# Performance work log

Hardware: AMD Instinct MI355X
Metric: run time of the kernel (lower is better)

## Reference

```python
import jax, jax.numpy as jnp
import numpy as np

B, L, D_MODEL = 4, 1024, 1024
S, NUM_TOKENS = 2048, 1000
H, E = 16, 256          # n_heads, d_keys
D_LLM = 4096


def setup_inputs() -> dict:
    key = jax.random.key(0)
    ks = jax.random.split(key, 11)
    def lin(k, fan_in, fan_out):
        bound = 1.0 / np.sqrt(fan_in)
        kw, kb = jax.random.split(k)
        W = jax.random.uniform(kw, (fan_out, fan_in), jnp.float32, -bound, bound)
        b = jax.random.uniform(kb, (fan_out,), jnp.float32, -bound, bound)
        return W, b
    Wq, bq = lin(ks[0], D_MODEL, H * E)
    Wk, bk = lin(ks[1], NUM_TOKENS, H * E)
    Wv, bv = lin(ks[2], NUM_TOKENS, H * E)
    Wo, bo = lin(ks[3], H * E, D_LLM)
    return {
        "target_embedding": jax.random.normal(ks[4], (B, L, D_MODEL), jnp.float32),
        "source_embedding": jax.random.normal(ks[5], (S, NUM_TOKENS), jnp.float32),
        "value_embedding": jax.random.normal(ks[6], (S, NUM_TOKENS), jnp.float32),
        "Wq": Wq, "bq": bq, "Wk": Wk, "bk": bk,
        "Wv": Wv, "bv": bv, "Wo": Wo, "bo": bo,
    }


def reference(target_embedding, source_embedding, value_embedding,
              Wq, bq, Wk, bk, Wv, bv, Wo, bo):
    # projections
    q = (target_embedding @ Wq.T + bq).reshape(B, L, H, E)   # [B,L,H,E]
    k = (source_embedding @ Wk.T + bk).reshape(S, H, E)      # [S,H,E] shared across batch
    v = (value_embedding @ Wv.T + bv).reshape(S, H, E)       # [S,H,E]
    scale = 1.0 / jnp.sqrt(jnp.float32(E))
    scores = jnp.einsum('blhe,she->bhls', q, k)               # [B,H,L,S]
    A = jax.nn.softmax(scale * scores, axis=-1)               # dropout is identity at eval
    out = jnp.einsum('bhls,she->blhe', A, v)                  # [B,L,H,E]
    out = out.reshape(B, L, H * E)
    return out @ Wo.T + bo                                    # [B,L,d_llm]
```

## Files before the change

kernel.cpp:

```cpp
#include <hip/hip_runtime.h>
#include <hip/hip_bf16.h>


#define B_ 4
#define L_ 1024
#define DM_ 1024
#define S_ 2048
#define NT_ 1000
#define H_ 16
#define E_ 256
#define HE_ 4096
#define DL_ 4096

typedef __attribute__((ext_vector_type(8))) short short8;
typedef __attribute__((ext_vector_type(4))) float f32x4;
typedef unsigned int u32;

__device__ __forceinline__ ushort f2bf(float x) {
  __hip_bfloat16 h = __float2bfloat16(x);
  return *reinterpret_cast<ushort*>(&h);
}

__device__ __forceinline__ void gload_lds16(const void* g, void* l) {
  __builtin_amdgcn_global_load_lds(
      (const __attribute__((address_space(1))) u32*)g,
      (__attribute__((address_space(3))) u32*)l, 16, 0, 0);
}

__global__ __launch_bounds__(256) void cast_pad_k(
    const float* __restrict__ src, ushort* __restrict__ dst,
    int rows, int ks, int kd) {
  const int kd8 = kd >> 3;
  const int idx = blockIdx.x * 256 + threadIdx.x;
  if (idx >= rows * kd8) return;
  const int r = idx / kd8;
  const int c0 = (idx - r * kd8) << 3;
  union { ushort u[8]; short8 v; } o;
  if (c0 + 8 <= ks) {
    const float4 f0 = *(const float4*)(src + (size_t)r * ks + c0);
    const float4 f1 = *(const float4*)(src + (size_t)r * ks + c0 + 4);
    o.u[0] = f2bf(f0.x); o.u[1] = f2bf(f0.y); o.u[2] = f2bf(f0.z); o.u[3] = f2bf(f0.w);
    o.u[4] = f2bf(f1.x); o.u[5] = f2bf(f1.y); o.u[6] = f2bf(f1.z); o.u[7] = f2bf(f1.w);
  } else {
#pragma unroll
    for (int j = 0; j < 8; ++j) o.u[j] = 0;
  }
  *(short8*)(dst + (size_t)r * kd + c0) = o.v;
}

template <typename OT>
__global__ __launch_bounds__(256) void gemm_mfma_t(
    const ushort* __restrict__ A, const ushort* __restrict__ W,
    const float* __restrict__ bias, OT* __restrict__ C,
    int M, int N, int K) {
  __shared__ char lds[2][2][16384];
  const int t = threadIdx.x;
  const int w = t >> 6;
  const int l = t & 63;
  const int a = l & 15;
  const int g = l >> 4;
  const int wr = w >> 1, wc = w & 1;
  const int bm = blockIdx.y << 7, bn = blockIdx.x << 7;
  const int sr = (l >> 3);
  const int sc = l & 7;

  f32x4 acc[4][4];
#pragma unroll
  for (int m = 0; m < 4; ++m)
#pragma unroll
    for (int n = 0; n < 4; ++n) acc[m][n] = (f32x4){0.f, 0.f, 0.f, 0.f};

  const int NTT = K >> 6;
  int cur = 0;

  auto stage = [&](int kt, int buf) {
    const int k0 = kt << 6;
#pragma unroll
    for (int j = 0; j < 4; ++j) {
      const int rb = (w << 5) + (j << 3);
      const int r = rb + sr;
      const int cs = sc ^ ((r & 4) >> 1);
      const size_t gofs = (size_t)r * K + k0 + (cs << 3);
      gload_lds16(A + (size_t)bm * K + gofs, &lds[buf][0][rb << 7]);
      gload_lds16(W + (size_t)bn * K + gofs, &lds[buf][1][rb << 7]);
    }
  };

  auto compute = [&](int buf) {
    const char* lA = lds[buf][0];
    const char* lB = lds[buf][1];
#pragma unroll
    for (int kk = 0; kk < 2; ++kk) {
      const int cc = (kk << 2) + g;
      short8 bfr[4];
#pragma unroll
      for (int n = 0; n < 4; ++n) {
        const int rl = (wc << 6) + (n << 4) + a;
        bfr[n] = *(const short8*)&lB[(rl << 7) + ((cc ^ ((rl & 4) >> 1)) << 4)];
      }
#pragma unroll
      for (int m = 0; m < 4; ++m) {
        const int rl = (wr << 6) + (m << 4) + a;
        const short8 afr = *(const short8*)&lA[(rl << 7) + ((cc ^ ((rl & 4) >> 1)) << 4)];
#pragma unroll
        for (int n = 0; n < 4; ++n)
          acc[m][n] = __builtin_amdgcn_mfma_f32_16x16x32_bf16(afr, bfr[n], acc[m][n], 0, 0, 0);
      }
    }
  };

  stage(0, 0);
  for (int kt = 0; kt < NTT; ++kt) {
    __syncthreads();
    if (kt + 1 < NTT) stage(kt + 1, cur ^ 1);
    compute(cur);
    cur ^= 1;
  }

  float bb[4];
#pragma unroll
  for (int n = 0; n < 4; ++n) bb[n] = bias[bn + (wc << 6) + (n << 4) + a];
#pragma unroll
  for (int m = 0; m < 4; ++m) {
#pragma unroll
    for (int ri = 0; ri < 4; ++ri) {
      const size_t row = (size_t)bm + (wr << 6) + (m << 4) + (g << 2) + ri;
      OT* Crow = C + row * N + bn + (wc << 6) + a;
#pragma unroll
      for (int n = 0; n < 4; ++n) {
        const float v = acc[m][n][ri] + bb[n];
        if constexpr (__is_same(OT, ushort)) Crow[n << 4] = f2bf(v);
        else Crow[n << 4] = v;
      }
    }
  }
}

__global__ __launch_bounds__(256) void transpose_bf16_k(
    const ushort* __restrict__ v, ushort* __restrict__ vt) {
  __shared__ ushort tile[64][72];
  const int t = threadIdx.x;
  const int s0 = blockIdx.x << 6;
  const int c0 = blockIdx.y << 6;
#pragma unroll
  for (int i = 0; i < 2; ++i) {
    const int idx = t + (i << 8);
    const int ch = idx & 7, s = idx >> 3;
    *(short8*)&tile[s][ch << 3] =
        *(const short8*)(v + (size_t)(s0 + s) * HE_ + c0 + (ch << 3));
  }
  __syncthreads();
#pragma unroll
  for (int i = 0; i < 2; ++i) {
    const int idx = t + (i << 8);
    const int sch = idx & 7, e = idx >> 3;
    union { ushort u[8]; short8 v8; } ou;
#pragma unroll
    for (int j = 0; j < 8; ++j) ou.u[j] = tile[(sch << 3) + j][e];
    *(short8*)(vt + (size_t)(c0 + e) * S_ + s0 + (sch << 3)) = ou.v8;
  }
}

__global__ __launch_bounds__(256) void attn_mfma_k(
    const ushort* __restrict__ q, const ushort* __restrict__ k,
    const ushort* __restrict__ vt, ushort* __restrict__ o) {
  __shared__ char kls[32 * 512];
  __shared__ char vls[256 * 64];
  __shared__ ushort pls[4][16 * 36];

  const int t = threadIdx.x;
  const int w = t >> 6;
  const int l = t & 63;
  const int a = l & 15;
  const int g = l >> 4;
  const int h = blockIdx.y;
  const int b = blockIdx.z;
  const size_t qrow = (size_t)(b << 10) + (blockIdx.x << 6) + (w << 4);

  short8 qf[8];
  {
    const size_t rb = (qrow + a) * HE_ + (h << 8) + (g << 3);
#pragma unroll
    for (int kk = 0; kk < 8; ++kk) qf[kk] = *(const short8*)(q + rb + (kk << 5));
  }

  f32x4 oa[16];
#pragma unroll
  for (int eg = 0; eg < 16; ++eg) oa[eg] = (f32x4){0.f, 0.f, 0.f, 0.f};
  float m_r[4] = {-3e38f, -3e38f, -3e38f, -3e38f};
  float l_r[4] = {0.f, 0.f, 0.f, 0.f};

  for (int s0 = 0; s0 < S_; s0 += 32) {
    __syncthreads();
#pragma unroll
    for (int i = 0; i < 4; ++i) {
      const int idx = t + (i << 8);
      const int c = idx & 31, s = idx >> 5;
      short8 kv = *(const short8*)(k + ((size_t)(s0 + s) << 12) + (h << 8) + (c << 3));
      *(short8*)&kls[((s << 9) + (c << 4)) ^ ((s & 7) << 4)] = kv;
    }
#pragma unroll
    for (int i = 0; i < 4; ++i) {
      const int idx = t + (i << 8);
      const int sc = idx & 3, e = idx >> 2;
      short8 vv = *(const short8*)(vt + ((size_t)((h << 8) + e) << 11) + s0 + (sc << 3));
      *(short8*)&vls[((e << 6) + (sc << 4)) ^ ((e & 3) << 4)] = vv;
    }
    __syncthreads();

    f32x4 sd0 = (f32x4){0.f, 0.f, 0.f, 0.f};
    f32x4 sd1 = (f32x4){0.f, 0.f, 0.f, 0.f};
#pragma unroll
    for (int kk = 0; kk < 8; ++kk) {
      const short8 kf0 = *(const short8*)
          &kls[((a << 9) + (g << 4) + (kk << 6)) ^ ((a & 7) << 4)];
      const short8 kf1 = *(const short8*)
          &kls[(((a + 16) << 9) + (g << 4) + (kk << 6)) ^ ((a & 7) << 4)];
      sd0 = __builtin_amdgcn_mfma_f32_16x16x32_bf16(qf[kk], kf0, sd0, 0, 0, 0);
      sd1 = __builtin_amdgcn_mfma_f32_16x16x32_bf16(qf[kk], kf1, sd1, 0, 0, 0);
    }

    float p0[4], p1[4];
#pragma unroll
    for (int r = 0; r < 4; ++r) {
      const float v0 = sd0[r] * 0.0625f;
      const float v1 = sd1[r] * 0.0625f;
      p0[r] = v0; p1[r] = v1;
      float mx = fmaxf(v0, v1);
      mx = fmaxf(mx, __shfl_xor(mx, 1));
      mx = fmaxf(mx, __shfl_xor(mx, 2));
      mx = fmaxf(mx, __shfl_xor(mx, 4));
      mx = fmaxf(mx, __shfl_xor(mx, 8));
      const float mnew = fmaxf(m_r[r], mx);
      const float corr = __expf(m_r[r] - mnew);
      m_r[r] = mnew;
      const float e0 = __expf(p0[r] - mnew);
      const float e1 = __expf(p1[r] - mnew);
      p0[r] = e0; p1[r] = e1;
      float sum = e0 + e1;
      sum += __shfl_xor(sum, 1);
      sum += __shfl_xor(sum, 2);
      sum += __shfl_xor(sum, 4);
      sum += __shfl_xor(sum, 8);
      l_r[r] = l_r[r] * corr + sum;
#pragma unroll
      for (int eg = 0; eg < 16; ++eg) oa[eg][r] *= corr;
    }

    {
      ushort* pw = pls[w];
#pragma unroll
      for (int r = 0; r < 4; ++r) {
        const int qq = (g << 2) + r;
        pw[qq * 36 + a] = f2bf(p0[r]);
        pw[qq * 36 + a + 16] = f2bf(p1[r]);
      }
    }
    asm volatile("s_waitcnt lgkmcnt(0)" ::: "memory");
    __builtin_amdgcn_sched_barrier(0);
    short8 pf;
    {
      const char* pb = (const char*)pls[w];
      union { unsigned long long u[2]; short8 v8; } pu;
      pu.u[0] = *(const unsigned long long*)(pb + a * 72 + (g << 4));
      pu.u[1] = *(const unsigned long long*)(pb + a * 72 + (g << 4) + 8);
      pf = pu.v8;
    }

#pragma unroll
    for (int eg = 0; eg < 16; ++eg) {
      const int e = (eg << 4) + a;
      const short8 vf = *(const short8*)
          &vls[((e << 6) + (g << 4)) ^ ((e & 3) << 4)];
      oa[eg] = __builtin_amdgcn_mfma_f32_16x16x32_bf16(pf, vf, oa[eg], 0, 0, 0);
    }
  }

  float inv[4];
#pragma unroll
  for (int r = 0; r < 4; ++r) inv[r] = 1.f / l_r[r];
#pragma unroll
  for (int eg = 0; eg < 16; ++eg) {
#pragma unroll
    for (int r = 0; r < 4; ++r) {
      o[(qrow + (g << 2) + r) * HE_ + (h << 8) + (eg << 4) + a] =
          f2bf(oa[eg][r] * inv[r]);
    }
  }
}

extern "C" void kernel_launch(void* const* d_in, const int* in_sizes, int n_in,
                              void* d_out, int out_size, void* d_ws, size_t ws_size,
                              hipStream_t stream) {
  (void)in_sizes; (void)n_in; (void)out_size; (void)ws_size;
  const float* te = (const float*)d_in[0];
  const float* se = (const float*)d_in[1];
  const float* ve = (const float*)d_in[2];
  const float* Wq = (const float*)d_in[3];
  const float* bq = (const float*)d_in[4];
  const float* Wk = (const float*)d_in[5];
  const float* bk = (const float*)d_in[6];
  const float* Wv = (const float*)d_in[7];
  const float* bv = (const float*)d_in[8];
  const float* Wo = (const float*)d_in[9];
  const float* bo = (const float*)d_in[10];
  float* out = (float*)d_out;

  ushort* tebf = (ushort*)d_ws;
  ushort* sebf = tebf + (size_t)4096 * 1024;
  ushort* vebf = sebf + (size_t)2048 * 1024;
  ushort* wqb  = vebf + (size_t)2048 * 1024;
  ushort* wkb  = wqb  + (size_t)4096 * 1024;
  ushort* wvb  = wkb  + (size_t)4096 * 1024;
  ushort* wob  = wvb  + (size_t)4096 * 1024;
  ushort* qbf  = wob  + (size_t)4096 * 4096;
  ushort* kbf  = qbf  + (size_t)4096 * 4096;
  ushort* vbf  = kbf  + (size_t)2048 * 4096;
  ushort* vtb  = vbf  + (size_t)2048 * 4096;
  ushort* awsb = vtb  + (size_t)4096 * 2048;

  dim3 blk(256);
  auto cgrid = [](int rows, int kd) { return dim3((rows * (kd >> 3) + 255) / 256); };
  cast_pad_k<<<cgrid(4096, 1024), blk, 0, stream>>>(te, tebf, 4096, 1024, 1024);
  cast_pad_k<<<cgrid(2048, 1024), blk, 0, stream>>>(se, sebf, 2048, 1000, 1024);
  cast_pad_k<<<cgrid(2048, 1024), blk, 0, stream>>>(ve, vebf, 2048, 1000, 1024);
  cast_pad_k<<<cgrid(4096, 1024), blk, 0, stream>>>(Wq, wqb, 4096, 1024, 1024);
  cast_pad_k<<<cgrid(4096, 1024), blk, 0, stream>>>(Wk, wkb, 4096, 1000, 1024);
  cast_pad_k<<<cgrid(4096, 1024), blk, 0, stream>>>(Wv, wvb, 4096, 1000, 1024);
  cast_pad_k<<<cgrid(4096, 4096), blk, 0, stream>>>(Wo, wob, 4096, 4096, 4096);

  gemm_mfma_t<ushort><<<dim3(32, 32), blk, 0, stream>>>(tebf, wqb, bq, qbf, 4096, 4096, 1024);
  gemm_mfma_t<ushort><<<dim3(32, 16), blk, 0, stream>>>(sebf, wkb, bk, kbf, 2048, 4096, 1024);
  gemm_mfma_t<ushort><<<dim3(32, 16), blk, 0, stream>>>(vebf, wvb, bv, vbf, 2048, 4096, 1024);
  transpose_bf16_k<<<dim3(S_ / 64, HE_ / 64), blk, 0, stream>>>(vbf, vtb);
  attn_mfma_k<<<dim3(L_ / 64, H_, B_), blk, 0, stream>>>(qbf, kbf, vtb, awsb);
  gemm_mfma_t<float><<<dim3(32, 32), blk, 0, stream>>>(awsb, wob, bo, out, 4096, 4096, 4096);
}
```

Before: 962.0 us.

## Widen attention KV tile to 64, use direct-to-LDS loads, lazy rescale, XCD-aware block mapping

The attention kernel now processes 64 keys per iteration instead of 32, halving the number of barrier-separated steps and doubling MFMA work per LDS fill. K and V tiles are loaded with global_load_lds using an XOR swizzle in place of register-staged copies. The online softmax skips rescaling the accumulators unless the running max grows by more than 8, which saves multiplies but leaves exponentials less tightly bounded. The 3D grid is flattened into a 1D index remapped so that blocks of the same head land on the same XCD, to improve L2 reuse of K/V. LDS usage doubles, which may reduce occupancy.

```diff
diff --git a/kernel.cpp b/kernel.cpp
--- a/kernel.cpp
+++ b/kernel.cpp
@@ -164,18 +164,21 @@
 __global__ __launch_bounds__(256) void attn_mfma_k(
     const ushort* __restrict__ q, const ushort* __restrict__ k,
     const ushort* __restrict__ vt, ushort* __restrict__ o) {
-  __shared__ char kls[32 * 512];
-  __shared__ char vls[256 * 64];
-  __shared__ ushort pls[4][16 * 36];
+  __shared__ char kls[64 * 512];
+  __shared__ char vls[256 * 128];
+  __shared__ ushort pls[4][16 * 72];
 
   const int t = threadIdx.x;
   const int w = t >> 6;
   const int l = t & 63;
   const int a = l & 15;
   const int g = l >> 4;
-  const int h = blockIdx.y;
-  const int b = blockIdx.z;
-  const size_t qrow = (size_t)(b << 10) + (blockIdx.x << 6) + (w << 4);
+  const int bid = blockIdx.x;
+  const int f = ((bid & 7) << 7) + (bid >> 3);
+  const int h = f >> 6;
+  const int bb = (f >> 4) & 3;
+  const int qt = f & 15;
+  const size_t qrow = ((size_t)bb << 10) + (qt << 6) + (w << 4);
 
   short8 qf[8];
   {
@@ -190,61 +193,70 @@
   float m_r[4] = {-3e38f, -3e38f, -3e38f, -3e38f};
   float l_r[4] = {0.f, 0.f, 0.f, 0.f};
 
-  for (int s0 = 0; s0 < S_; s0 += 32) {
+  for (int s0 = 0; s0 < S_; s0 += 64) {
     __syncthreads();
 #pragma unroll
-    for (int i = 0; i < 4; ++i) {
-      const int idx = t + (i << 8);
-      const int c = idx & 31, s = idx >> 5;
-      short8 kv = *(const short8*)(k + ((size_t)(s0 + s) << 12) + (h << 8) + (c << 3));
-      *(short8*)&kls[((s << 9) + (c << 4)) ^ ((s & 7) << 4)] = kv;
-    }
-#pragma unroll
-    for (int i = 0; i < 4; ++i) {
-      const int idx = t + (i << 8);
-      const int sc = idx & 3, e = idx >> 2;
-      short8 vv = *(const short8*)(vt + ((size_t)((h << 8) + e) << 11) + s0 + (sc << 3));
-      *(short8*)&vls[((e << 6) + (sc << 4)) ^ ((e & 3) << 4)] = vv;
+    for (int j = 0; j < 8; ++j) {
+      const int srow = ((j << 2) + w) << 1;
+      const int s = srow + (l >> 5);
+      const int c = l & 31;
+      gload_lds16(k + ((size_t)(s0 + s) << 12) + (h << 8) + ((c ^ (s & 7)) << 3),
+                  &kls[srow << 9]);
+    }
+#pragma unroll
+    for (int j = 0; j < 8; ++j) {
+      const int ebase = ((j << 2) + w) << 3;
+      const int e = ebase + (l >> 3);
+      const int c = l & 7;
+      gload_lds16(vt + ((size_t)((h << 8) + e) << 11) + s0 + ((c ^ (e & 7)) << 3),
+                  &vls[ebase << 7]);
     }
     __syncthreads();
 
-    f32x4 sd0 = (f32x4){0.f, 0.f, 0.f, 0.f};
-    f32x4 sd1 = (f32x4){0.f, 0.f, 0.f, 0.f};
+    f32x4 sd[4];
+#pragma unroll
+    for (int si = 0; si < 4; ++si) sd[si] = (f32x4){0.f, 0.f, 0.f, 0.f};
 #pragma unroll
     for (int kk = 0; kk < 8; ++kk) {
-      const short8 kf0 = *(const short8*)
-          &kls[((a << 9) + (g << 4) + (kk << 6)) ^ ((a & 7) << 4)];
-      const short8 kf1 = *(const short8*)
-          &kls[(((a + 16) << 9) + (g << 4) + (kk << 6)) ^ ((a & 7) << 4)];
-      sd0 = __builtin_amdgcn_mfma_f32_16x16x32_bf16(qf[kk], kf0, sd0, 0, 0, 0);
-      sd1 = __builtin_amdgcn_mfma_f32_16x16x32_bf16(qf[kk], kf1, sd1, 0, 0, 0);
-    }
-
-    float p0[4], p1[4];
+#pragma unroll
+      for (int si = 0; si < 4; ++si) {
+        const int srow = a + (si << 4);
+        const short8 kf = *(const short8*)
+            &kls[(srow << 9) + ((((kk << 2) + g) ^ (srow & 7)) << 4)];
+        sd[si] = __builtin_amdgcn_mfma_f32_16x16x32_bf16(qf[kk], kf, sd[si], 0, 0, 0);
+      }
+    }
+
+    float pe[4][4];
+    const float scl = 0.0625f;
 #pragma unroll
     for (int r = 0; r < 4; ++r) {
-      const float v0 = sd0[r] * 0.0625f;
-      const float v1 = sd1[r] * 0.0625f;
-      p0[r] = v0; p1[r] = v1;
-      float mx = fmaxf(v0, v1);
+      const float v0 = sd[0][r] * scl, v1 = sd[1][r] * scl;
+      const float v2 = sd[2][r] * scl, v3 = sd[3][r] * scl;
+      float mx = fmaxf(fmaxf(v0, v1), fmaxf(v2, v3));
       mx = fmaxf(mx, __shfl_xor(mx, 1));
       mx = fmaxf(mx, __shfl_xor(mx, 2));
       mx = fmaxf(mx, __shfl_xor(mx, 4));
       mx = fmaxf(mx, __shfl_xor(mx, 8));
-      const float mnew = fmaxf(m_r[r], mx);
-      const float corr = __expf(m_r[r] - mnew);
-      m_r[r] = mnew;
-      const float e0 = __expf(p0[r] - mnew);
-      const float e1 = __expf(p1[r] - mnew);
-      p0[r] = e0; p1[r] = e1;
-      float sum = e0 + e1;
+      if (__any(mx > m_r[r] + 8.f)) {
+        const float mnew = fmaxf(m_r[r], mx);
+        const float corr = __expf(m_r[r] - mnew);
+        m_r[r] = mnew;
+        l_r[r] *= corr;
+#pragma unroll
+        for (int eg = 0; eg < 16; ++eg) oa[eg][r] *= corr;
+      }
+      const float e0 = __expf(v0 - m_r[r]);
+      const float e1 = __expf(v1 - m_r[r]);
+      const float e2 = __expf(v2 - m_r[r]);
+      const float e3 = __expf(v3 - m_r[r]);
+      float sum = (e0 + e1) + (e2 + e3);
       sum += __shfl_xor(sum, 1);
       sum += __shfl_xor(sum, 2);
       sum += __shfl_xor(sum, 4);
       sum += __shfl_xor(sum, 8);
-      l_r[r] = l_r[r] * corr + sum;
-#pragma unroll
-      for (int eg = 0; eg < 16; ++eg) oa[eg][r] *= corr;
+      l_r[r] += sum;
+      pe[0][r] = e0; pe[1][r] = e1; pe[2][r] = e2; pe[3][r] = e3;
     }
 
     {
@@ -252,27 +264,26 @@
 #pragma unroll
       for (int r = 0; r < 4; ++r) {
         const int qq = (g << 2) + r;
-        pw[qq * 36 + a] = f2bf(p0[r]);
-        pw[qq * 36 + a + 16] = f2bf(p1[r]);
+#pragma unroll
+        for (int si = 0; si < 4; ++si)
+          pw[qq * 72 + (si << 4) + a] = f2bf(pe[si][r]);
       }
     }
     asm volatile("s_waitcnt lgkmcnt(0)" ::: "memory");
     __builtin_amdgcn_sched_barrier(0);
-    short8 pf;
-    {
-      const char* pb = (const char*)pls[w];
-      union { unsigned long long u[2]; short8 v8; } pu;
-      pu.u[0] = *(const unsigned long long*)(pb + a * 72 + (g << 4));
-      pu.u[1] = *(const unsigned long long*)(pb + a * 72 + (g << 4) + 8);
-      pf = pu.v8;
-    }
+    const char* pb = (const char*)pls[w];
+    const short8 pf0 = *(const short8*)(pb + a * 144 + (g << 4));
+    const short8 pf1 = *(const short8*)(pb + a * 144 + 64 + (g << 4));
 
 #pragma unroll
     for (int eg = 0; eg < 16; ++eg) {
       const int e = (eg << 4) + a;
-      const short8 vf = *(const short8*)
-          &vls[((e << 6) + (g << 4)) ^ ((e & 3) << 4)];
-      oa[eg] = __builtin_amdgcn_mfma_f32_16x16x32_bf16(pf, vf, oa[eg], 0, 0, 0);
+      const short8 vf0 = *(const short8*)
+          &vls[(e << 7) + ((g ^ (e & 7)) << 4)];
+      const short8 vf1 = *(const short8*)
+          &vls[(e << 7) + (((4 + g) ^ (e & 7)) << 4)];
+      oa[eg] = __builtin_amdgcn_mfma_f32_16x16x32_bf16(pf0, vf0, oa[eg], 0, 0, 0);
+      oa[eg] = __builtin_amdgcn_mfma_f32_16x16x32_bf16(pf1, vf1, oa[eg], 0, 0, 0);
     }
   }
 
@@ -333,6 +344,6 @@
   gemm_mfma_t<ushort><<<dim3(32, 16), blk, 0, stream>>>(sebf, wkb, bk, kbf, 2048, 4096, 1024);
   gemm_mfma_t<ushort><<<dim3(32, 16), blk, 0, stream>>>(vebf, wvb, bv, vbf, 2048, 4096, 1024);
   transpose_bf16_k<<<dim3(S_ / 64, HE_ / 64), blk, 0, stream>>>(vbf, vtb);
-  attn_mfma_k<<<dim3(L_ / 64, H_, B_), blk, 0, stream>>>(qbf, kbf, vtb, awsb);
+  attn_mfma_k<<<dim3(1024), blk, 0, stream>>>(qbf, kbf, vtb, awsb);
   gemm_mfma_t<float><<<dim3(32, 32), blk, 0, stream>>>(awsb, wob, bo, out, 4096, 4096, 4096);
 }
```

Result: faster. 797.2 us (-17.1%).
